# Kernel optimization log

Hardware: AMD Instinct MI355X
Metric: run time of the kernel (lower is better)

The kernel has to match this reference:

```python
import jax, jax.numpy as jnp
import numpy as np

EPS = 1e-6

def rms_norm(x):
    # RMSNorm, affine=False
    return x * jax.lax.rsqrt(jnp.mean(x * x, axis=-1, keepdims=True) + EPS)

def apply_rope(x, cos, sin):
    # x: [N, T, h, d], cos/sin: [T, d//2], half-split rotation
    x1, x2 = jnp.split(x, 2, axis=-1)
    c = cos[None, :, None, :]
    s = sin[None, :, None, :]
    return jnp.concatenate([x1 * c - x2 * s, x1 * s + x2 * c], axis=-1)

def setup_inputs() -> dict:
    key = jax.random.key(0)
    k0, k1, k2 = jax.random.split(key, 3)
    N, T, D, hd = 1, 2048, 2048, 128
    input_NTD = jax.random.normal(k0, (N, T, D), jnp.float32)
    qkv_weight = jax.random.normal(k1, (3, D, D), jnp.float32) / np.sqrt(D) / 2.0
    o_weight = jax.random.normal(k2, (D, D), jnp.float32) * 0.02
    # standard 1d RoPE angle table
    pos = jnp.arange(T, dtype=jnp.float32)
    inv_freq = 1.0 / (10000.0 ** (jnp.arange(hd // 2, dtype=jnp.float32) / (hd // 2)))
    ang = pos[:, None] * inv_freq[None, :]  # [T, hd//2]
    return {
        "input_NTD": input_NTD,
        "qkv_weight": qkv_weight,
        "o_weight": o_weight,
        "cos": jnp.cos(ang),
        "sin": jnp.sin(ang),
    }

def reference(input_NTD, qkv_weight, o_weight, cos, sin):
    N, T, D = input_NTD.shape
    hd = cos.shape[-1] * 2
    h = D // hd
    w = qkv_weight.reshape(3 * D, D)
    qkv = rms_norm(input_NTD) @ w.T                      # [N, T, 3D]
    qkv = qkv.reshape(N, T, 3 * h, hd)
    q, k, v = jnp.split(qkv, 3, axis=2)                  # each [N, T, h, hd]
    q = apply_rope(rms_norm(q), cos, sin)
    k = apply_rope(rms_norm(k), cos, sin)
    scale = 1.0 / np.sqrt(hd)
    scores = jnp.einsum('nqhd,nkhd->nhqk', q, k) * scale  # [N, h, T, T]
    causal = jnp.tril(jnp.ones((T, T), bool))
    scores = jnp.where(causal[None, None], scores, -jnp.inf)
    att = jax.nn.softmax(scores, axis=-1)
    x = jnp.einsum('nhqk,nkhd->nqhd', att, v).reshape(N, T, D)
    out = input_NTD + x @ o_weight.T
    return out, k, v
```

## Files before the change

kernel.cpp:

```cpp
#include <hip/hip_runtime.h>
#include <hip/hip_bf16.h>

typedef unsigned short u16;
typedef unsigned int u32;
typedef __bf16 bf16x8 __attribute__((ext_vector_type(8)));
typedef u16 u16x8 __attribute__((ext_vector_type(8)));
typedef u16 u16x4 __attribute__((ext_vector_type(4)));
typedef float f32x4 __attribute__((ext_vector_type(4)));

#define T_SEQ 2048
#define DMODEL 2048
#define NHEAD 16
#define HDIM 128
#define ATT_SCALE 0.08838834764831843f

__device__ __forceinline__ u16 f2bf(float f) {
    return __builtin_bit_cast(u16, __float2bfloat16(f));
}
__device__ __forceinline__ bf16x8 as_bf(u16x8 v) {
    return __builtin_bit_cast(bf16x8, v);
}
__device__ __forceinline__ float lo2f(u32 w) { return __builtin_bit_cast(float, w << 16); }
__device__ __forceinline__ float hi2f(u32 w) { return __builtin_bit_cast(float, w & 0xffff0000u); }
__device__ __forceinline__ void gload_lds16(const u16* g, u16* l) {
    __builtin_amdgcn_global_load_lds(
        (const __attribute__((address_space(1))) u32*)(g),
        (__attribute__((address_space(3))) u32*)(l), 16, 0, 0);
}

__global__ __launch_bounds__(256) void cast_both(const float* __restrict__ w1,
                                                 const float* __restrict__ w2,
                                                 u16* __restrict__ d1,
                                                 u16* __restrict__ d2) {
    int i = blockIdx.x * 256 + threadIdx.x;
    const float* src; u16* dst; int k;
    if (i < 1572864) { src = w1; dst = d1; k = i; }
    else             { src = w2; dst = d2; k = i - 1572864; }
    float4 a = ((const float4*)src)[2 * k];
    float4 b = ((const float4*)src)[2 * k + 1];
    u16x8 o;
    o[0] = f2bf(a.x); o[1] = f2bf(a.y); o[2] = f2bf(a.z); o[3] = f2bf(a.w);
    o[4] = f2bf(b.x); o[5] = f2bf(b.y); o[6] = f2bf(b.z); o[7] = f2bf(b.w);
    *(u16x8*)(dst + (size_t)k * 8) = o;
}

__global__ __launch_bounds__(256) void rmsnorm_row(const float* __restrict__ x,
                                                   u16* __restrict__ xn) {
    const int row = blockIdx.x, tid = threadIdx.x;
    const float* xr = x + (size_t)row * DMODEL;
    float4 a = ((const float4*)xr)[2 * tid];
    float4 b = ((const float4*)xr)[2 * tid + 1];
    float ss = a.x*a.x + a.y*a.y + a.z*a.z + a.w*a.w
             + b.x*b.x + b.y*b.y + b.z*b.z + b.w*b.w;
#pragma unroll
    for (int off = 32; off; off >>= 1) ss += __shfl_xor(ss, off);
    __shared__ float red[4];
    if ((tid & 63) == 0) red[tid >> 6] = ss;
    __syncthreads();
    float tot = red[0] + red[1] + red[2] + red[3];
    float r = rsqrtf(tot * (1.f / DMODEL) + 1e-6f);
    u16x8 o;
    o[0] = f2bf(a.x*r); o[1] = f2bf(a.y*r); o[2] = f2bf(a.z*r); o[3] = f2bf(a.w*r);
    o[4] = f2bf(b.x*r); o[5] = f2bf(b.y*r); o[6] = f2bf(b.z*r); o[7] = f2bf(b.w*r);
    *(u16x8*)(xn + (size_t)row * DMODEL + tid * 8) = o;
}

#define VM4 asm volatile("s_waitcnt vmcnt(4)" ::: "memory");
#define VM0 asm volatile("s_waitcnt vmcnt(0)" ::: "memory");

#define ENDP                                                                  \
  __builtin_amdgcn_s_barrier();                                               \
  __builtin_amdgcn_sched_barrier(0);

#define LDA(BUF, MH)                                                          \
  _Pragma("unroll") for (int mq = 0; mq < 4; ++mq) {                          \
    int ra = wr + (MH) * 64 + mq * 16 + fr;                                   \
    int sw = ra & 7;                                                          \
    _Pragma("unroll") for (int k2 = 0; k2 < 2; ++k2)                          \
      av[mq][k2] = *(const u16x8*)(sA[BUF] + ra * 64 +                        \
                                   ((((k2 << 2) | fg) ^ sw) << 3));           \
  }

#define LDB(BUF, NH)                                                          \
  _Pragma("unroll") for (int nq = 0; nq < 2; ++nq) {                          \
    int rb = wc + (NH) * 32 + nq * 16 + fr;                                   \
    int sw = rb & 7;                                                          \
    _Pragma("unroll") for (int k2 = 0; k2 < 2; ++k2)                          \
      bv[nq][k2] = *(const u16x8*)(sB[BUF] + rb * 64 +                        \
                                   ((((k2 << 2) | fg) ^ sw) << 3));           \
  }

#define MFMAQ(MH, NH)                                                         \
  __builtin_amdgcn_s_barrier();                                               \
  __builtin_amdgcn_s_setprio(1);                                              \
  _Pragma("unroll") for (int k2 = 0; k2 < 2; ++k2)                            \
    _Pragma("unroll") for (int mq = 0; mq < 4; ++mq)                          \
      _Pragma("unroll") for (int nq = 0; nq < 2; ++nq)                        \
        acc[(MH) * 4 + mq][(NH) * 2 + nq] =                                   \
            __builtin_amdgcn_mfma_f32_16x16x32_bf16(                          \
                as_bf(av[mq][k2]), as_bf(bv[nq][k2]),                         \
                acc[(MH) * 4 + mq][(NH) * 2 + nq], 0, 0, 0);                  \
  __builtin_amdgcn_s_setprio(0);

__global__ __launch_bounds__(512) void gemm256(const u16* __restrict__ A,
                                               const u16* __restrict__ B,
                                               u16* __restrict__ C,
                                               int M, int N, int K) {
    extern __shared__ char smem[];
    const int tid = threadIdx.x, lane = tid & 63, wid = tid >> 6;
    const int bm = blockIdx.y * 256, bn = blockIdx.x * 256;
    const int wr = (wid >> 2) * 128, wc = (wid & 3) * 64;
    const int fr = lane & 15, fg = lane >> 4;

    u16* sA[2] = {(u16*)smem, (u16*)(smem + 65536)};
    u16* sB[2] = {(u16*)(smem + 32768), (u16*)(smem + 98304)};

    const int cs = (((tid & 7) ^ ((tid >> 3) & 7)) << 3);
    const int s8 = (tid & 7) << 3;
    const int rr6 = tid >> 3;
    const int rb0 = ((tid >> 8) << 6) + ((tid >> 3) & 31);

    auto stA = [&](int buf, int k0, int mh) {
#pragma unroll
        for (int j = 0; j < 2; ++j) {
            int r = j * 128 + mh * 64 + rr6;
            gload_lds16(A + (size_t)(bm + r) * K + k0 + cs, sA[buf] + r * 64 + s8);
        }
    };
    auto stB = [&](int buf, int k0, int nh) {
#pragma unroll
        for (int j = 0; j < 2; ++j) {
            int r = j * 128 + nh * 32 + rb0;
            gload_lds16(B + (size_t)(bn + r) * K + k0 + cs, sB[buf] + r * 64 + s8);
        }
    };

    f32x4 acc[8][4] = {};
    u16x8 av[4][2], bv[2][2];
    const int nt = K >> 6;

    stA(0, 0, 0); stA(0, 0, 1); stB(0, 0, 0); stB(0, 0, 1);
    stA(1, 64, 0); stB(1, 64, 1);
    VM4
    __builtin_amdgcn_s_barrier();
    __builtin_amdgcn_sched_barrier(0);

    for (int it = 0; it < (nt >> 1); ++it) {
        const int kc = it << 7;
        const int kn1 = kc + 64, kn2 = kc + 128, kn3 = kc + 192;
        const bool st2 = (kn2 < K), st3 = (kn3 < K);

        LDA(0, 0) LDB(0, 0)
        stA(1, kn1, 1);
        MFMAQ(0, 0) ENDP
        LDB(0, 1)
        stB(1, kn1, 0);
        MFMAQ(0, 1) ENDP
        LDA(0, 1)
        if (st2) stA(0, kn2, 0);
        MFMAQ(1, 1) ENDP
        LDB(0, 0)
        if (st2) stB(0, kn2, 1);
        MFMAQ(1, 0)
        if (st2) { VM4 } else { VM0 }
        ENDP
        LDA(1, 0) LDB(1, 0)
        if (st2) stA(0, kn2, 1);
        MFMAQ(0, 0) ENDP
        LDB(1, 1)
        if (st2) stB(0, kn2, 0);
        MFMAQ(0, 1) ENDP
        LDA(1, 1)
        if (st3) stA(1, kn3, 0);
        MFMAQ(1, 1) ENDP
        LDB(1, 0)
        if (st3) stB(1, kn3, 1);
        MFMAQ(1, 0)
        VM4
        ENDP
    }

#pragma unroll
    for (int am = 0; am < 8; ++am)
#pragma unroll
        for (int bq = 0; bq < 4; ++bq)
#pragma unroll
            for (int r = 0; r < 4; ++r) {
                int row = bm + wr + am * 16 + fg * 4 + r;
                int col = bn + wc + bq * 16 + fr;
                C[(size_t)row * N + col] = f2bf(acc[am][bq][r]);
            }
}

#define LDAH(BUF, MH)                                                         \
  _Pragma("unroll") for (int mq = 0; mq < 2; ++mq) {                          \
    int ra = wr + (MH) * 32 + mq * 16 + fr;                                   \
    int sw = ra & 7;                                                          \
    _Pragma("unroll") for (int k2 = 0; k2 < 2; ++k2)                          \
      av[mq][k2] = *(const u16x8*)(sA[BUF] + ra * 64 +                        \
                                   ((((k2 << 2) | fg) ^ sw) << 3));           \
  }

#define LDBH(BUF, NH)                                                         \
  _Pragma("unroll") for (int nq = 0; nq < 2; ++nq) {                          \
    int rb = wc + (NH) * 32 + nq * 16 + fr;                                   \
    int sw = rb & 7;                                                          \
    _Pragma("unroll") for (int k2 = 0; k2 < 2; ++k2)                          \
      bv[nq][k2] = *(const u16x8*)(sB[BUF] + rb * 64 +                        \
                                   ((((k2 << 2) | fg) ^ sw) << 3));           \
  }

#define MFMAQH(MH, NH)                                                        \
  __builtin_amdgcn_s_barrier();                                               \
  __builtin_amdgcn_s_setprio(1);                                              \
  _Pragma("unroll") for (int k2 = 0; k2 < 2; ++k2)                            \
    _Pragma("unroll") for (int mq = 0; mq < 2; ++mq)                          \
      _Pragma("unroll") for (int nq = 0; nq < 2; ++nq)                        \
        acc[(MH) * 2 + mq][(NH) * 2 + nq] =                                   \
            __builtin_amdgcn_mfma_f32_16x16x32_bf16(                          \
                as_bf(av[mq][k2]), as_bf(bv[nq][k2]),                         \
                acc[(MH) * 2 + mq][(NH) * 2 + nq], 0, 0, 0);                  \
  __builtin_amdgcn_s_setprio(0);

__global__ __launch_bounds__(256) void gemm128(const u16* __restrict__ A,
                                               const u16* __restrict__ B,
                                               float* __restrict__ C,
                                               const float* __restrict__ resid,
                                               int M, int N, int K) {
    extern __shared__ char smem[];
    const int tid = threadIdx.x, lane = tid & 63, wid = tid >> 6;
    const int bm = blockIdx.y * 128, bn = blockIdx.x * 128;
    const int wr = (wid >> 1) * 64, wc = (wid & 1) * 64;
    const int fr = lane & 15, fg = lane >> 4;

    u16* sA[2] = {(u16*)smem, (u16*)(smem + 32768)};
    u16* sB[2] = {(u16*)(smem + 16384), (u16*)(smem + 49152)};

    const int cs = (((tid & 7) ^ ((tid >> 3) & 7)) << 3);
    const int s8 = (tid & 7) << 3;
    const int rr5 = tid >> 3;

    auto stA = [&](int buf, int k0, int mh) {
#pragma unroll
        for (int j = 0; j < 2; ++j) {
            int r = j * 64 + mh * 32 + rr5;
            gload_lds16(A + (size_t)(bm + r) * K + k0 + cs, sA[buf] + r * 64 + s8);
        }
    };
    auto stB = [&](int buf, int k0, int nh) {
#pragma unroll
        for (int j = 0; j < 2; ++j) {
            int r = j * 64 + nh * 32 + rr5;
            gload_lds16(B + (size_t)(bn + r) * K + k0 + cs, sB[buf] + r * 64 + s8);
        }
    };

    f32x4 acc[4][4] = {};
    u16x8 av[2][2], bv[2][2];
    const int nt = K >> 6;

    stA(0, 0, 0); stA(0, 0, 1); stB(0, 0, 0); stB(0, 0, 1);
    stA(1, 64, 0); stB(1, 64, 1);
    VM4
    __builtin_amdgcn_s_barrier();
    __builtin_amdgcn_sched_barrier(0);

    for (int it = 0; it < (nt >> 1); ++it) {
        const int kc = it << 7;
        const int kn1 = kc + 64, kn2 = kc + 128, kn3 = kc + 192;
        const bool st2 = (kn2 < K), st3 = (kn3 < K);

        LDAH(0, 0) LDBH(0, 0)
        stA(1, kn1, 1);
        MFMAQH(0, 0) ENDP
        LDBH(0, 1)
        stB(1, kn1, 0);
        MFMAQH(0, 1) ENDP
        LDAH(0, 1)
        if (st2) stA(0, kn2, 0);
        MFMAQH(1, 1) ENDP
        LDBH(0, 0)
        if (st2) stB(0, kn2, 1);
        MFMAQH(1, 0)
        if (st2) { VM4 } else { VM0 }
        ENDP
        LDAH(1, 0) LDBH(1, 0)
        if (st2) stA(0, kn2, 1);
        MFMAQH(0, 0) ENDP
        LDBH(1, 1)
        if (st2) stB(0, kn2, 0);
        MFMAQH(0, 1) ENDP
        LDAH(1, 1)
        if (st3) stA(1, kn3, 0);
        MFMAQH(1, 1) ENDP
        LDBH(1, 0)
        if (st3) stB(1, kn3, 1);
        MFMAQH(1, 0)
        VM4
        ENDP
    }

#pragma unroll
    for (int am = 0; am < 4; ++am)
#pragma unroll
        for (int bq = 0; bq < 4; ++bq)
#pragma unroll
            for (int r = 0; r < 4; ++r) {
                int row = bm + wr + am * 16 + fg * 4 + r;
                int col = bn + wc + bq * 16 + fr;
                float val = acc[am][bq][r] + resid[(size_t)row * N + col];
                C[(size_t)row * N + col] = val;
            }
}

__global__ __launch_bounds__(256) void rope_split(const u16* __restrict__ qkv,
                                                  const float* __restrict__ cosb,
                                                  const float* __restrict__ sinb,
                                                  u16* __restrict__ q_bf,
                                                  u16* __restrict__ k_bf,
                                                  float* __restrict__ k_out,
                                                  float* __restrict__ v_out) {
    const int t = blockIdx.x, tid = threadIdx.x, wid = tid >> 6, lane = tid & 63;
    const u16* row = qkv + (size_t)t * (3 * DMODEL);
    const int dp = (lane & 31) << 1;
    float2 c2 = *(const float2*)(cosb + t * 64 + dp);
    float2 s2 = *(const float2*)(sinb + t * 64 + dp);
    const bool hi = lane >= 32;

    for (int task = wid; task < 32; task += 4) {
        u32 w = *(const u32*)(row + task * 128 + lane * 2);
        float xa = lo2f(w), xb = hi2f(w);
        float ss = xa * xa + xb * xb;
#pragma unroll
        for (int off = 32; off; off >>= 1) ss += __shfl_xor(ss, off);
        float rn = rsqrtf(ss * (1.f / 128.f) + 1e-6f);
        float pa = __shfl_xor(xa, 32), pb = __shfl_xor(xb, 32);
        float oa, ob;
        if (!hi) {
            oa = (xa * c2.x - pa * s2.x) * rn;
            ob = (xb * c2.y - pb * s2.y) * rn;
        } else {
            oa = (pa * s2.x + xa * c2.x) * rn;
            ob = (pb * s2.y + xb * c2.y) * rn;
        }
        u32 pk = (u32)f2bf(oa) | ((u32)f2bf(ob) << 16);
        if (task < 16) {
            *(u32*)(q_bf + ((size_t)task * T_SEQ + t) * 128 + lane * 2) = pk;
        } else {
            int hh = task - 16;
            *(u32*)(k_bf + ((size_t)hh * T_SEQ + t) * 128 + lane * 2) = pk;
            float2 kk; kk.x = oa; kk.y = ob;
            *(float2*)(k_out + (size_t)t * DMODEL + hh * 128 + lane * 2) = kk;
        }
    }
    {
        u16x8 vv = *(const u16x8*)(row + 2 * DMODEL + tid * 8);
        float4 f0, f1;
        f0.x = __builtin_bit_cast(float, (u32)vv[0] << 16);
        f0.y = __builtin_bit_cast(float, (u32)vv[1] << 16);
        f0.z = __builtin_bit_cast(float, (u32)vv[2] << 16);
        f0.w = __builtin_bit_cast(float, (u32)vv[3] << 16);
        f1.x = __builtin_bit_cast(float, (u32)vv[4] << 16);
        f1.y = __builtin_bit_cast(float, (u32)vv[5] << 16);
        f1.z = __builtin_bit_cast(float, (u32)vv[6] << 16);
        f1.w = __builtin_bit_cast(float, (u32)vv[7] << 16);
        *(float4*)(v_out + (size_t)t * DMODEL + tid * 8) = f0;
        *(float4*)(v_out + (size_t)t * DMODEL + tid * 8 + 4) = f1;
    }
}

__global__ __launch_bounds__(256) void vtrans(const u16* __restrict__ qkv,
                                              u16* __restrict__ vt) {
    const int b = blockIdx.x, tid = threadIdx.x;
    const int head = b >> 7;
    const int i = (b & 127) * 256 + tid;
    const int d = i & 127, tc = i >> 7;
    u16x8 o;
#pragma unroll
    for (int j = 0; j < 8; ++j)
        o[j] = qkv[(size_t)(tc * 8 + j) * (3 * DMODEL) + 2 * DMODEL + head * 128 + d];
    *(u16x8*)&vt[((size_t)head * 128 + d) * T_SEQ + tc * 8] = o;
}

__global__ __launch_bounds__(256) void attn_fwd(const u16* __restrict__ qb,
                                                const u16* __restrict__ kb,
                                                const u16* __restrict__ vtb,
                                                u16* __restrict__ xout) {
    __shared__ u16 Ks[2][64 * 128];
    __shared__ u16 Vs[2][128 * 64];
    __shared__ u16 Ps[4][16 * 64];

    const int bid = blockIdx.x;
    const int r8 = bid & 7, s = bid >> 3;
    const int head = r8 + ((s >> 5) << 3);
    const int j = s & 31;
    const int qt = (s < 32) ? (31 - j) : j;

    const int tid = threadIdx.x, wid = tid >> 6, lane = tid & 63;
    const int fr = lane & 15, fg = lane >> 4;
    const u16* kh = kb + (size_t)head * T_SEQ * 128;
    const u16* vth = vtb + (size_t)head * 128 * T_SEQ;
    const u16* qh = qb + (size_t)head * T_SEQ * 128;
    const int q0 = qt * 64 + wid * 16;
    const int qrow_g = q0 + fr;

    u16x8 bq[4];
    {
        const u16* qrow = qh + (size_t)(q0 + fr) * 128 + fg * 8;
#pragma unroll
        for (int cc = 0; cc < 4; ++cc) bq[cc] = *(const u16x8*)(qrow + cc * 32);
    }

    auto stage = [&](int kv0, int buf) {
#pragma unroll
        for (int i = 0; i < 4; ++i) {
            int idx = i * 256 + tid;
            int r = idx >> 4;
            int cbs = ((idx & 15) << 4) ^ ((r & 7) << 4);
            gload_lds16(kh + (size_t)(kv0 + r) * 128 + (cbs >> 1), &Ks[buf][idx * 8]);
        }
#pragma unroll
        for (int i = 0; i < 4; ++i) {
            int idx = i * 256 + tid;
            int d = idx >> 3;
            int cbs = ((idx & 7) << 4) ^ ((d & 7) << 4);
            gload_lds16(vth + (size_t)d * T_SEQ + kv0 + (cbs >> 1), &Vs[buf][idx * 8]);
        }
    };

    stage(0, 0);

    f32x4 o[8] = {};
    float m_run = -1e30f, l_run = 0.f;
    const int nt = qt + 1;

    for (int kt = 0; kt < nt; ++kt) {
        const int kv0 = kt * 64;
        const int buf = kt & 1;
        if (kt + 1 < nt) {
            stage(kv0 + 64, buf ^ 1);
            asm volatile("s_waitcnt vmcnt(8)" ::: "memory");
        } else {
            asm volatile("s_waitcnt vmcnt(0)" ::: "memory");
        }
        __builtin_amdgcn_s_barrier();
        __builtin_amdgcn_sched_barrier(0);

        const char* ksb = (const char*)&Ks[buf][0];
        const char* vsb = (const char*)&Vs[buf][0];
        char* psb = (char*)&Ps[wid][0];

        float p[4][4];
        float mx = -1e30f;
        const bool diag = (kv0 + 64 > q0);
#pragma unroll
        for (int st = 0; st < 4; ++st) {
            f32x4 sacc = {0.f, 0.f, 0.f, 0.f};
#pragma unroll
            for (int c4 = 0; c4 < 4; ++c4) {
                int r = st * 16 + fr;
                int cb = c4 * 64 + fg * 16;
                u16x8 ak = *(const u16x8*)(ksb + r * 256 + (cb ^ ((r & 7) << 4)));
                sacc = __builtin_amdgcn_mfma_f32_16x16x32_bf16(
                    as_bf(ak), as_bf(bq[c4]), sacc, 0, 0, 0);
            }
#pragma unroll
            for (int rr = 0; rr < 4; ++rr) {
                float sv = sacc[rr] * ATT_SCALE;
                if (diag) {
                    int kvg = kv0 + st * 16 + fg * 4 + rr;
                    sv = (kvg <= qrow_g) ? sv : -1e30f;
                }
                p[st][rr] = sv;
                mx = fmaxf(mx, sv);
            }
        }
        mx = fmaxf(mx, __shfl_xor(mx, 16));
        mx = fmaxf(mx, __shfl_xor(mx, 32));

        if (__all(mx - m_run <= 8.f)) {
            float rs = 0.f;
#pragma unroll
            for (int st = 0; st < 4; ++st) {
                u16x4 pw;
#pragma unroll
                for (int rr = 0; rr < 4; ++rr) {
                    float e = __expf(p[st][rr] - m_run);
                    rs += e;
                    pw[rr] = f2bf(e);
                }
                *(u16x4*)(psb + fr * 128 + ((st * 32 + fg * 8) ^ ((fr & 7) << 4))) = pw;
            }
            rs += __shfl_xor(rs, 16);
            rs += __shfl_xor(rs, 32);
            l_run += rs;
        } else {
            float m_new = fmaxf(m_run, mx);
            float corr = __expf(m_run - m_new);
            float rs = 0.f;
#pragma unroll
            for (int st = 0; st < 4; ++st) {
                u16x4 pw;
#pragma unroll
                for (int rr = 0; rr < 4; ++rr) {
                    float e = __expf(p[st][rr] - m_new);
                    rs += e;
                    pw[rr] = f2bf(e);
                }
                *(u16x4*)(psb + fr * 128 + ((st * 32 + fg * 8) ^ ((fr & 7) << 4))) = pw;
            }
            rs += __shfl_xor(rs, 16);
            rs += __shfl_xor(rs, 32);
            l_run = l_run * corr + rs;
            m_run = m_new;
            float ct[4];
#pragma unroll
            for (int rr = 0; rr < 4; ++rr) ct[rr] = __shfl(corr, fg * 4 + rr);
#pragma unroll
            for (int f = 0; f < 8; ++f)
#pragma unroll
                for (int rr = 0; rr < 4; ++rr) o[f][rr] *= ct[rr];
        }

#pragma unroll
        for (int ks = 0; ks < 2; ++ks) {
            u16x8 pa = *(const u16x8*)(psb + fr * 128 + ((ks * 64 + fg * 16) ^ ((fr & 7) << 4)));
#pragma unroll
            for (int f = 0; f < 8; ++f) {
                int d = f * 16 + fr;
                u16x8 vB = *(const u16x8*)(vsb + d * 128 + ((ks * 64 + fg * 16) ^ ((d & 7) << 4)));
                o[f] = __builtin_amdgcn_mfma_f32_16x16x32_bf16(
                    as_bf(pa), as_bf(vB), o[f], 0, 0, 0);
            }
        }
        __builtin_amdgcn_s_barrier();
    }

    float li[4];
#pragma unroll
    for (int rr = 0; rr < 4; ++rr) li[rr] = __shfl(l_run, fg * 4 + rr);
#pragma unroll
    for (int f = 0; f < 8; ++f)
#pragma unroll
        for (int rr = 0; rr < 4; ++rr) {
            int trow = q0 + fg * 4 + rr;
            float val = o[f][rr] / li[rr];
            xout[(size_t)trow * DMODEL + head * 128 + f * 16 + fr] = f2bf(val);
        }
}

extern "C" void kernel_launch(void* const* d_in, const int* in_sizes, int n_in,
                              void* d_out, int out_size, void* d_ws, size_t ws_size,
                              hipStream_t stream) {
    const float* x_in = (const float*)d_in[0];
    const float* w_qkv = (const float*)d_in[1];
    const float* w_o = (const float*)d_in[2];
    const float* cosb = (const float*)d_in[3];
    const float* sinb = (const float*)d_in[4];

    float* out = (float*)d_out;
    float* k_out = out + 4194304;
    float* v_out = out + 8388608;

    char* ws = (char*)d_ws;
    u16* xn    = (u16*)(ws);
    u16* w_bf  = (u16*)(ws + (size_t)(8u << 20));
    u16* o_bf  = (u16*)(ws + (size_t)(32u << 20));
    u16* qkv   = (u16*)(ws + (size_t)(40u << 20));
    u16* q_bf  = (u16*)(ws + (size_t)(64u << 20));
    u16* k_bf  = (u16*)(ws + (size_t)(72u << 20));
    u16* vt_bf = (u16*)(ws + (size_t)(80u << 20));
    u16* x_bf  = (u16*)(ws + (size_t)(88u << 20));

    (void)hipFuncSetAttribute(reinterpret_cast<const void*>(&gemm256),
                              hipFuncAttributeMaxDynamicSharedMemorySize, 131072);
    (void)hipFuncSetAttribute(reinterpret_cast<const void*>(&gemm128),
                              hipFuncAttributeMaxDynamicSharedMemorySize, 65536);

    cast_both<<<8192, 256, 0, stream>>>(w_qkv, w_o, w_bf, o_bf);
    rmsnorm_row<<<2048, 256, 0, stream>>>(x_in, xn);
    gemm256<<<dim3(24, 8), 512, 131072, stream>>>(xn, w_bf, qkv, 2048, 6144, 2048);
    rope_split<<<2048, 256, 0, stream>>>(qkv, cosb, sinb, q_bf, k_bf, k_out, v_out);
    vtrans<<<2048, 256, 0, stream>>>(qkv, vt_bf);
    attn_fwd<<<512, 256, 0, stream>>>(q_bf, k_bf, vt_bf, x_bf);
    gemm128<<<dim3(16, 16), 256, 65536, stream>>>(x_bf, o_bf, out, x_in, 2048, 2048, 2048);
}
```

Baseline: 189.1 us.

## Retile QKV GEMM to 256x192 blocks and use exp2 softmax in attention

The QKV projection GEMM changes from 256x256 to 256x192 tiles, so the grid grows from 192 to 256 blocks, which matches the 256 CUs and removes the partial second wave. The B-tile load schedule, register fragments, LDS layout and vmcnt waits are reworked for the narrower tile. Separately, attention folds log2(e) into the score scale and uses exp2f instead of __expf, with the rescale threshold adjusted to match. The smaller tile reuses each A tile less, and the new pipeline schedule needs its waitcnt accounting to be correct.

```diff
diff --git a/kernel.cpp b/kernel.cpp
--- a/kernel.cpp
+++ b/kernel.cpp
@@ -12,7 +12,7 @@
 #define DMODEL 2048
 #define NHEAD 16
 #define HDIM 128
-#define ATT_SCALE 0.08838834764831843f
+#define ATT_SCALE_L2E 0.12751744f
 
 __device__ __forceinline__ u16 f2bf(float f) {
     return __builtin_bit_cast(u16, __float2bfloat16(f));
@@ -65,6 +65,7 @@
     *(u16x8*)(xn + (size_t)row * DMODEL + tid * 8) = o;
 }
 
+#define VM2 asm volatile("s_waitcnt vmcnt(2)" ::: "memory");
 #define VM4 asm volatile("s_waitcnt vmcnt(4)" ::: "memory");
 #define VM0 asm volatile("s_waitcnt vmcnt(0)" ::: "memory");
 
@@ -72,7 +73,7 @@
   __builtin_amdgcn_s_barrier();                                               \
   __builtin_amdgcn_sched_barrier(0);
 
-#define LDA(BUF, MH)                                                          \
+#define LDA192(BUF, MH)                                                       \
   _Pragma("unroll") for (int mq = 0; mq < 4; ++mq) {                          \
     int ra = wr + (MH) * 64 + mq * 16 + fr;                                   \
     int sw = ra & 7;                                                          \
@@ -81,44 +82,61 @@
                                    ((((k2 << 2) | fg) ^ sw) << 3));           \
   }
 
-#define LDB(BUF, NH)                                                          \
+#define LDB0_192(BUF)                                                         \
   _Pragma("unroll") for (int nq = 0; nq < 2; ++nq) {                          \
-    int rb = wc + (NH) * 32 + nq * 16 + fr;                                   \
+    int rb = wc + nq * 16 + fr;                                               \
     int sw = rb & 7;                                                          \
     _Pragma("unroll") for (int k2 = 0; k2 < 2; ++k2)                          \
       bv[nq][k2] = *(const u16x8*)(sB[BUF] + rb * 64 +                        \
                                    ((((k2 << 2) | fg) ^ sw) << 3));           \
   }
 
-#define MFMAQ(MH, NH)                                                         \
+#define LDB1_192(BUF)                                                         \
+  {                                                                           \
+    int rb = wc + 32 + fr;                                                    \
+    int sw = rb & 7;                                                          \
+    _Pragma("unroll") for (int k2 = 0; k2 < 2; ++k2)                          \
+      bv1[k2] = *(const u16x8*)(sB[BUF] + rb * 64 +                           \
+                                ((((k2 << 2) | fg) ^ sw) << 3));              \
+  }
+
+#define MFMAQ_N0(MH)                                                          \
   __builtin_amdgcn_s_barrier();                                               \
   __builtin_amdgcn_s_setprio(1);                                              \
   _Pragma("unroll") for (int k2 = 0; k2 < 2; ++k2)                            \
     _Pragma("unroll") for (int mq = 0; mq < 4; ++mq)                          \
       _Pragma("unroll") for (int nq = 0; nq < 2; ++nq)                        \
-        acc[(MH) * 4 + mq][(NH) * 2 + nq] =                                   \
-            __builtin_amdgcn_mfma_f32_16x16x32_bf16(                          \
-                as_bf(av[mq][k2]), as_bf(bv[nq][k2]),                         \
-                acc[(MH) * 4 + mq][(NH) * 2 + nq], 0, 0, 0);                  \
+        acc[(MH) * 4 + mq][nq] = __builtin_amdgcn_mfma_f32_16x16x32_bf16(     \
+            as_bf(av[mq][k2]), as_bf(bv[nq][k2]), acc[(MH) * 4 + mq][nq],     \
+            0, 0, 0);                                                         \
   __builtin_amdgcn_s_setprio(0);
 
-__global__ __launch_bounds__(512) void gemm256(const u16* __restrict__ A,
+#define MFMAQ_N1(MH)                                                          \
+  __builtin_amdgcn_s_barrier();                                               \
+  __builtin_amdgcn_s_setprio(1);                                              \
+  _Pragma("unroll") for (int k2 = 0; k2 < 2; ++k2)                            \
+    _Pragma("unroll") for (int mq = 0; mq < 4; ++mq)                          \
+      acc[(MH) * 4 + mq][2] = __builtin_amdgcn_mfma_f32_16x16x32_bf16(        \
+          as_bf(av[mq][k2]), as_bf(bv1[k2]), acc[(MH) * 4 + mq][2],           \
+          0, 0, 0);                                                           \
+  __builtin_amdgcn_s_setprio(0);
+
+__global__ __launch_bounds__(512) void gemm192(const u16* __restrict__ A,
                                                const u16* __restrict__ B,
                                                u16* __restrict__ C,
                                                int M, int N, int K) {
     extern __shared__ char smem[];
     const int tid = threadIdx.x, lane = tid & 63, wid = tid >> 6;
-    const int bm = blockIdx.y * 256, bn = blockIdx.x * 256;
-    const int wr = (wid >> 2) * 128, wc = (wid & 3) * 64;
+    const int bm = blockIdx.y * 256, bn = blockIdx.x * 192;
+    const int wr = (wid >> 2) * 128, wc = (wid & 3) * 48;
     const int fr = lane & 15, fg = lane >> 4;
 
-    u16* sA[2] = {(u16*)smem, (u16*)(smem + 65536)};
-    u16* sB[2] = {(u16*)(smem + 32768), (u16*)(smem + 98304)};
+    u16* sA[2] = {(u16*)smem, (u16*)(smem + 57344)};
+    u16* sB[2] = {(u16*)(smem + 32768), (u16*)(smem + 90112)};
 
     const int cs = (((tid & 7) ^ ((tid >> 3) & 7)) << 3);
     const int s8 = (tid & 7) << 3;
     const int rr6 = tid >> 3;
-    const int rb0 = ((tid >> 8) << 6) + ((tid >> 3) & 31);
 
     auto stA = [&](int buf, int k0, int mh) {
 #pragma unroll
@@ -127,21 +145,18 @@
             gload_lds16(A + (size_t)(bm + r) * K + k0 + cs, sA[buf] + r * 64 + s8);
         }
     };
-    auto stB = [&](int buf, int k0, int nh) {
-#pragma unroll
-        for (int j = 0; j < 2; ++j) {
-            int r = j * 128 + nh * 32 + rb0;
-            gload_lds16(B + (size_t)(bn + r) * K + k0 + cs, sB[buf] + r * 64 + s8);
-        }
+    auto stB = [&](int buf, int k0, int bt) {
+        int r = bt * 64 + rr6;
+        gload_lds16(B + (size_t)(bn + r) * K + k0 + cs, sB[buf] + r * 64 + s8);
     };
 
-    f32x4 acc[8][4] = {};
-    u16x8 av[4][2], bv[2][2];
+    f32x4 acc[8][3] = {};
+    u16x8 av[4][2], bv[2][2], bv1[2];
     const int nt = K >> 6;
 
-    stA(0, 0, 0); stA(0, 0, 1); stB(0, 0, 0); stB(0, 0, 1);
-    stA(1, 64, 0); stB(1, 64, 1);
-    VM4
+    stA(0, 0, 0); stA(0, 0, 1); stB(0, 0, 0); stB(0, 0, 1); stB(0, 0, 2);
+    stA(1, 64, 0);
+    VM2
     __builtin_amdgcn_s_barrier();
     __builtin_amdgcn_sched_barrier(0);
 
@@ -150,40 +165,38 @@
         const int kn1 = kc + 64, kn2 = kc + 128, kn3 = kc + 192;
         const bool st2 = (kn2 < K), st3 = (kn3 < K);
 
-        LDA(0, 0) LDB(0, 0)
-        stA(1, kn1, 1);
-        MFMAQ(0, 0) ENDP
-        LDB(0, 1)
-        stB(1, kn1, 0);
-        MFMAQ(0, 1) ENDP
-        LDA(0, 1)
+        LDA192(0, 0) LDB0_192(0)
+        stA(1, kn1, 1); stB(1, kn1, 0);
+        MFMAQ_N0(0) ENDP
+        LDB1_192(0)
+        stB(1, kn1, 1); stB(1, kn1, 2);
+        MFMAQ_N1(0) ENDP
+        LDA192(0, 1)
         if (st2) stA(0, kn2, 0);
-        MFMAQ(1, 1) ENDP
-        LDB(0, 0)
-        if (st2) stB(0, kn2, 1);
-        MFMAQ(1, 0)
-        if (st2) { VM4 } else { VM0 }
+        MFMAQ_N1(1) ENDP
+        LDB0_192(0)
+        MFMAQ_N0(1)
+        if (st2) { VM2 } else { VM0 }
         ENDP
-        LDA(1, 0) LDB(1, 0)
-        if (st2) stA(0, kn2, 1);
-        MFMAQ(0, 0) ENDP
-        LDB(1, 1)
-        if (st2) stB(0, kn2, 0);
-        MFMAQ(0, 1) ENDP
-        LDA(1, 1)
+        LDA192(1, 0) LDB0_192(1)
+        if (st2) { stA(0, kn2, 1); stB(0, kn2, 0); }
+        MFMAQ_N0(0) ENDP
+        LDB1_192(1)
+        if (st2) { stB(0, kn2, 1); stB(0, kn2, 2); }
+        MFMAQ_N1(0) ENDP
+        LDA192(1, 1)
         if (st3) stA(1, kn3, 0);
-        MFMAQ(1, 1) ENDP
-        LDB(1, 0)
-        if (st3) stB(1, kn3, 1);
-        MFMAQ(1, 0)
-        VM4
+        MFMAQ_N1(1) ENDP
+        LDB0_192(1)
+        MFMAQ_N0(1)
+        if (st3) { VM2 } else { VM0 }
         ENDP
     }
 
 #pragma unroll
     for (int am = 0; am < 8; ++am)
 #pragma unroll
-        for (int bq = 0; bq < 4; ++bq)
+        for (int bq = 0; bq < 3; ++bq)
 #pragma unroll
             for (int r = 0; r < 4; ++r) {
                 int row = bm + wr + am * 16 + fg * 4 + r;
@@ -466,7 +479,7 @@
             }
 #pragma unroll
             for (int rr = 0; rr < 4; ++rr) {
-                float sv = sacc[rr] * ATT_SCALE;
+                float sv = sacc[rr] * ATT_SCALE_L2E;
                 if (diag) {
                     int kvg = kv0 + st * 16 + fg * 4 + rr;
                     sv = (kvg <= qrow_g) ? sv : -1e30f;
@@ -478,14 +491,14 @@
         mx = fmaxf(mx, __shfl_xor(mx, 16));
         mx = fmaxf(mx, __shfl_xor(mx, 32));
 
-        if (__all(mx - m_run <= 8.f)) {
+        if (__all(mx - m_run <= 11.5f)) {
             float rs = 0.f;
 #pragma unroll
             for (int st = 0; st < 4; ++st) {
                 u16x4 pw;
 #pragma unroll
                 for (int rr = 0; rr < 4; ++rr) {
-                    float e = __expf(p[st][rr] - m_run);
+                    float e = exp2f(p[st][rr] - m_run);
                     rs += e;
                     pw[rr] = f2bf(e);
                 }
@@ -496,14 +509,14 @@
             l_run += rs;
         } else {
             float m_new = fmaxf(m_run, mx);
-            float corr = __expf(m_run - m_new);
+            float corr = exp2f(m_run - m_new);
             float rs = 0.f;
 #pragma unroll
             for (int st = 0; st < 4; ++st) {
                 u16x4 pw;
 #pragma unroll
                 for (int rr = 0; rr < 4; ++rr) {
-                    float e = __expf(p[st][rr] - m_new);
+                    float e = exp2f(p[st][rr] - m_new);
                     rs += e;
                     pw[rr] = f2bf(e);
                 }
@@ -572,14 +585,14 @@
     u16* vt_bf = (u16*)(ws + (size_t)(80u << 20));
     u16* x_bf  = (u16*)(ws + (size_t)(88u << 20));
 
-    (void)hipFuncSetAttribute(reinterpret_cast<const void*>(&gemm256),
-                              hipFuncAttributeMaxDynamicSharedMemorySize, 131072);
+    (void)hipFuncSetAttribute(reinterpret_cast<const void*>(&gemm192),
+                              hipFuncAttributeMaxDynamicSharedMemorySize, 114688);
     (void)hipFuncSetAttribute(reinterpret_cast<const void*>(&gemm128),
                               hipFuncAttributeMaxDynamicSharedMemorySize, 65536);
 
     cast_both<<<8192, 256, 0, stream>>>(w_qkv, w_o, w_bf, o_bf);
     rmsnorm_row<<<2048, 256, 0, stream>>>(x_in, xn);
-    gemm256<<<dim3(24, 8), 512, 131072, stream>>>(xn, w_bf, qkv, 2048, 6144, 2048);
+    gemm192<<<dim3(32, 8), 512, 114688, stream>>>(xn, w_bf, qkv, 2048, 6144, 2048);
     rope_split<<<2048, 256, 0, stream>>>(qkv, cosb, sinb, q_bf, k_bf, k_out, v_out);
     vtrans<<<2048, 256, 0, stream>>>(qkv, vt_bf);
     attn_fwd<<<512, 256, 0, stream>>>(q_bf, k_bf, vt_bf, x_bf);
```

Result: no change. 185.4 us (-1.9%).
